# Optimization experiments

Hardware: AMD Instinct MI355X
Metric: run time of the kernel (lower is better)

Reference implementation:

```python
import jax, jax.numpy as jnp
import numpy as np

BETA = 0.25
NUM_CODES = 8192
DIM_LATENT = 256
BATCH = 32768


def setup_inputs() -> dict:
    key = jax.random.key(0)
    k1, k2 = jax.random.split(key)
    z_e = jax.random.normal(k1, (BATCH, DIM_LATENT), dtype=jnp.float32)
    # nn.init.uniform_(codebook.weight, -1/num_codes, 1/num_codes)
    codebook = jax.random.uniform(
        k2, (NUM_CODES, DIM_LATENT), dtype=jnp.float32,
        minval=-1.0 / NUM_CODES, maxval=1.0 / NUM_CODES,
    )
    return {"z_e": z_e, "codebook": codebook}


def reference(z_e, codebook):
    # squared L2 distances via the ||z||^2 + ||e||^2 - 2 z.e expansion
    z2 = jnp.sum(z_e * z_e, axis=1, keepdims=True)          # [B, 1]
    e2 = jnp.sum(codebook * codebook, axis=1)[None, :]       # [1, K]
    ze = jnp.einsum('bd,kd->bk', z_e, codebook)              # [B, K]
    dist = z2 + e2 - 2.0 * ze                                # [B, K]
    indices = jnp.argmin(dist, axis=1)                       # [B]
    z_q = codebook[indices]                                  # [B, d] gather

    cb_loss = jnp.mean((z_q - jax.lax.stop_gradient(z_e)) ** 2)
    commit_loss = jnp.mean((z_e - jax.lax.stop_gradient(z_q)) ** 2)
    vq_loss = cb_loss + BETA * commit_loss

    # straight-through estimator
    z_q_st = z_e + jax.lax.stop_gradient(z_q - z_e)
    return (z_q_st, indices, vq_loss, cb_loss, commit_loss)
```

## Files before the change

### kernel.cpp

```cpp
#include <hip/hip_runtime.h>

#define BATCH   32768
#define DIM     256
#define NCODES  8192
#define BETA    0.25f
#define EPS     3e-4f
#define CAND_CAP 128

typedef unsigned short ushort_t;
typedef unsigned char  uchar_t;
typedef unsigned long long u64;
typedef __attribute__((ext_vector_type(8))) short bf16x8;
typedef __attribute__((ext_vector_type(4))) float f32x4;

#define GLOAD16(gp, lp) __builtin_amdgcn_global_load_lds( \
    (const __attribute__((address_space(1))) void*)(gp), \
    (__attribute__((address_space(3))) void*)(lp), 16, 0, 0)

__device__ inline ushort_t f2bf(float f) {
    union { float f; unsigned u; } v; v.f = f;
    return (ushort_t)((v.u + 0x7FFF + ((v.u >> 16) & 1)) >> 16);
}
__device__ inline ushort_t f2bf_rd(float f) {
    union { float f; unsigned u; } v; v.f = f;
    unsigned u = v.u;
    if (f < 0.0f) u += 0xFFFFu;
    return (ushort_t)(u >> 16);
}

__global__ void vq_prep_kernel(const float* __restrict__ z,
                               const float* __restrict__ cb,
                               float* __restrict__ e2, float* __restrict__ z2,
                               ushort_t* __restrict__ eh, ushort_t* __restrict__ zh,
                               float* __restrict__ loss_acc) {
    const int lane = threadIdx.x & 63;
    const int wid  = threadIdx.x >> 6;
    const int item = blockIdx.x * 4 + wid;
    const float* src;
    ushort_t* dst;
    if (item < NCODES) { src = cb + (size_t)item * DIM;            dst = eh + (size_t)item * DIM; }
    else               { src = z  + (size_t)(item - NCODES) * DIM; dst = zh + (size_t)(item - NCODES) * DIM; }
    const float4 v = *(const float4*)(src + lane * 4);
    ushort4 b; b.x = f2bf(v.x); b.y = f2bf(v.y); b.z = f2bf(v.z); b.w = f2bf(v.w);
    *(ushort4*)(dst + lane * 4) = b;
    float s = v.x * v.x + v.y * v.y + v.z * v.z + v.w * v.w;
    #pragma unroll
    for (int off = 32; off > 0; off >>= 1) s += __shfl_down(s, off, 64);
    if (lane == 0) {
        if (item < NCODES) e2[item] = s;
        else               z2[item - NCODES] = s;
    }
    if (blockIdx.x == 0 && threadIdx.x == 0) *loss_acc = 0.0f;
}

__launch_bounds__(512, 2)
__global__ void vq_screen_kernel(const ushort_t* __restrict__ zh_g,
                                 const ushort_t* __restrict__ eh_g,
                                 const float* __restrict__ e2g,
                                 ushort_t* __restrict__ tilemin_g,
                                 uchar_t* __restrict__ mask_g) {
    __shared__ ushort_t zh_s[2][8 * 512];
    __shared__ ushort_t eh_s[2][32 * 512];

    const int t    = threadIdx.x;
    const int w    = t >> 6;
    const int lane = t & 63;
    const int c    = lane & 15;
    const int q    = lane >> 4;
    const int h    = w >> 2;
    const int cq   = w & 3;
    const int row0 = blockIdx.x * 128;

    #define STAGE(n_, b_) do {                                                 \
        const int ct_ = (n_) >> 3;                                             \
        const int kc_ = ((n_) & 7) * 32;                                       \
        GLOAD16(zh_g + (size_t)(row0 + w * 16 + (lane >> 2)) * DIM + kc_ + (lane & 3) * 8, \
                &zh_s[b_][w * 512]);                                           \
        _Pragma("unroll")                                                      \
        for (int s_ = 0; s_ < 4; ++s_) {                                       \
            const int c16_ = w * 4 + s_;                                       \
            GLOAD16(eh_g + (size_t)(ct_ * 512 + c16_ * 16 + (lane >> 2)) * DIM + kc_ + (lane & 3) * 8, \
                    &eh_s[b_][c16_ * 512]);                                    \
        }                                                                      \
    } while (0)

    STAGE(0, 0);

    f32x4 acc[4][8];
    for (int n = 0; n < 128; ++n) {
        const int kc_i = n & 7;
        if (kc_i == 0) {
            #pragma unroll
            for (int i = 0; i < 4; ++i)
                #pragma unroll
                for (int j = 0; j < 8; ++j) acc[i][j] = (f32x4)0.0f;
        }
        __syncthreads();
        if (n < 127) STAGE(n + 1, (n + 1) & 1);
        const int b = n & 1;

        bf16x8 a[4], bfr[8];
        #pragma unroll
        for (int i = 0; i < 4; ++i)
            a[i] = *(const bf16x8*)&zh_s[b][(h * 4 + i) * 512 + c * 32 + q * 8];
        #pragma unroll
        for (int j = 0; j < 8; ++j)
            bfr[j] = *(const bf16x8*)&eh_s[b][(cq * 8 + j) * 512 + c * 32 + q * 8];
        #pragma unroll
        for (int i = 0; i < 4; ++i)
            #pragma unroll
            for (int j = 0; j < 8; ++j)
                acc[i][j] = __builtin_amdgcn_mfma_f32_16x16x32_bf16(a[i], bfr[j], acc[i][j], 0, 0, 0);

        if (kc_i == 7) {
            const int ct = n >> 3;
            float e2v[8];
            #pragma unroll
            for (int j = 0; j < 8; ++j) e2v[j] = e2g[ct * 512 + cq * 128 + j * 16 + c];

            float tm[4][4];
            #pragma unroll
            for (int i = 0; i < 4; ++i)
                #pragma unroll
                for (int reg = 0; reg < 4; ++reg) tm[i][reg] = 3.4e38f;
            #pragma unroll
            for (int i = 0; i < 4; ++i)
                #pragma unroll
                for (int j = 0; j < 8; ++j)
                    #pragma unroll
                    for (int reg = 0; reg < 4; ++reg) {
                        const float s = fmaf(-2.0f, acc[i][j][reg], e2v[j]);
                        acc[i][j][reg] = s;
                        tm[i][reg] = fminf(tm[i][reg], s);
                    }
            #pragma unroll
            for (int st = 1; st < 16; st <<= 1)
                #pragma unroll
                for (int i = 0; i < 4; ++i)
                    #pragma unroll
                    for (int reg = 0; reg < 4; ++reg)
                        tm[i][reg] = fminf(tm[i][reg], __shfl_xor(tm[i][reg], st, 64));

            const int tile = ct * 4 + cq;
            #pragma unroll
            for (int i = 0; i < 4; ++i)
                #pragma unroll
                for (int reg = 0; reg < 4; ++reg) {
                    const int row = row0 + h * 64 + i * 16 + q * 4 + reg;
                    const float thr = tm[i][reg] + EPS;
                    unsigned m8 = 0;
                    #pragma unroll
                    for (int j = 0; j < 8; ++j)
                        m8 |= (unsigned)(acc[i][j][reg] <= thr) << j;
                    mask_g[(size_t)row * 1024 + tile * 16 + c] = (uchar_t)m8;
                    if (c == 0) tilemin_g[(size_t)row * 64 + tile] = f2bf_rd(tm[i][reg]);
                }
        }
    }
    #undef STAGE
}

__device__ inline u64 vq_eval(const float* zrow, const float* __restrict__ cb,
                              const float* __restrict__ e2g, float z2v, int code) {
    const float4* z4 = (const float4*)zrow;
    const float4* e4 = (const float4*)(cb + (size_t)code * DIM);
    float acc = 0.0f;
    #pragma unroll 8
    for (int k4 = 0; k4 < DIM / 4; ++k4) {
        const float4 a = z4[k4];
        const float4 b = e4[k4];
        acc = fmaf(a.x, b.x, acc);
        acc = fmaf(a.y, b.y, acc);
        acc = fmaf(a.z, b.z, acc);
        acc = fmaf(a.w, b.w, acc);
    }
    const float S  = z2v + e2g[code];
    const float sc = fmaf(-2.0f, acc, S);
    union { float f; unsigned u; } sb; sb.f = sc;
    return ((u64)sb.u << 32) | (unsigned)code;
}

__global__ void vq_select_kernel(const float* __restrict__ z,
                                 const float* __restrict__ cb,
                                 const float* __restrict__ e2g,
                                 const float* __restrict__ z2g,
                                 const ushort_t* __restrict__ tilemin_g,
                                 const uchar_t* __restrict__ mask_g,
                                 float* __restrict__ idx_f,
                                 int* __restrict__ idx_i) {
    __shared__ float    zrow_s[4][DIM];
    __shared__ ushort_t cand_s[4][CAND_CAP];

    const int lane = threadIdx.x & 63;
    const int w    = threadIdx.x >> 6;
    const int row  = blockIdx.x * 4 + w;

    *(float4*)&zrow_s[w][lane * 4] = *(const float4*)(z + (size_t)row * DIM + lane * 4);

    union { unsigned u; float f; } tv;
    tv.u = ((unsigned)tilemin_g[(size_t)row * 64 + lane]) << 16;
    const float tm = tv.f;
    float gmin = tm;
    #pragma unroll
    for (int d = 32; d > 0; d >>= 1) gmin = fminf(gmin, __shfl_xor(gmin, d, 64));
    const float thr = gmin + EPS;

    u64 m0 = 0, m1 = 0;
    if (tm <= thr) {
        const uchar_t* mb = mask_g + (size_t)row * 1024 + lane * 16;
        m0 = *(const u64*)(mb);
        m1 = *(const u64*)(mb + 8);
    }
    const unsigned cnt = __popcll(m0) + __popcll(m1);
    unsigned inc = cnt;
    #pragma unroll
    for (int d = 1; d < 64; d <<= 1) {
        const unsigned o = __shfl_up(inc, d, 64);
        if (lane >= d) inc += o;
    }
    const unsigned excl  = inc - cnt;
    const unsigned total = __shfl(inc, 63, 64);
    const float z2v = z2g[row];
    u64 best = ~0ull;

    __syncthreads();

    unsigned slot = excl;
    while (m0) {
        const int p = __builtin_ctzll(m0); m0 &= m0 - 1;
        const unsigned code = lane * 128 + (p & 7) * 16 + (p >> 3);
        if (slot < CAND_CAP) cand_s[w][slot] = (ushort_t)code;
        else best = min(best, vq_eval(zrow_s[w], cb, e2g, z2v, (int)code));
        ++slot;
    }
    while (m1) {
        const int p = __builtin_ctzll(m1); m1 &= m1 - 1;
        const unsigned code = lane * 128 + (p & 7) * 16 + 8 + (p >> 3);
        if (slot < CAND_CAP) cand_s[w][slot] = (ushort_t)code;
        else best = min(best, vq_eval(zrow_s[w], cb, e2g, z2v, (int)code));
        ++slot;
    }

    __syncthreads();

    const int n = (int)(total < CAND_CAP ? total : CAND_CAP);
    for (int s = lane; s < n; s += 64)
        best = min(best, vq_eval(zrow_s[w], cb, e2g, z2v, (int)cand_s[w][s]));

    #pragma unroll
    for (int d = 32; d > 0; d >>= 1) {
        const u64 o = (u64)__shfl_xor((unsigned long long)best, d, 64);
        best = min(best, o);
    }
    if (lane == 0) {
        const int k = (int)(best & (u64)(NCODES - 1));
        idx_f[row] = (float)k;
        idx_i[row] = k;
    }
}

__global__ void vq_gather_loss_kernel(const float* __restrict__ z,
                                      const float* __restrict__ cb,
                                      const int* __restrict__ idx_i,
                                      float* __restrict__ zq_out,
                                      float* __restrict__ loss_acc) {
    const int lane = threadIdx.x & 63;
    const int wid  = threadIdx.x >> 6;
    const int row  = blockIdx.x * 4 + wid;
    const int k = idx_i[row];
    const float4 e  = *(const float4*)(cb + (size_t)k * DIM + lane * 4);
    const float4 zv = *(const float4*)(z + (size_t)row * DIM + lane * 4);
    const float dx = e.x - zv.x, dy = e.y - zv.y, dz = e.z - zv.z, dw = e.w - zv.w;
    float4 o;
    o.x = zv.x + dx; o.y = zv.y + dy; o.z = zv.z + dz; o.w = zv.w + dw;
    *(float4*)(zq_out + (size_t)row * DIM + lane * 4) = o;
    float s = dx * dx + dy * dy + dz * dz + dw * dw;
    #pragma unroll
    for (int off = 32; off > 0; off >>= 1) s += __shfl_down(s, off, 64);
    __shared__ float wsum[4];
    if (lane == 0) wsum[wid] = s;
    __syncthreads();
    if (threadIdx.x == 0)
        atomicAdd(loss_acc, wsum[0] + wsum[1] + wsum[2] + wsum[3]);
}

__global__ void vq_finalize_kernel(const float* __restrict__ loss_acc,
                                   float* __restrict__ out_losses) {
    const float mean = *loss_acc * (1.0f / (float)(BATCH * DIM));
    out_losses[0] = mean + BETA * mean;
    out_losses[1] = mean;
    out_losses[2] = mean;
}

extern "C" void kernel_launch(void* const* d_in, const int* in_sizes, int n_in,
                              void* d_out, int out_size, void* d_ws, size_t ws_size,
                              hipStream_t stream) {
    const float* z  = (const float*)d_in[0];
    const float* cb = (const float*)d_in[1];

    float* out    = (float*)d_out;
    float* zq     = out;
    float* idx_f  = out + (size_t)BATCH * DIM;
    float* losses = out + (size_t)BATCH * DIM + BATCH;
    uchar_t* mask = (uchar_t*)d_out;

    float*    ws        = (float*)d_ws;
    float*    loss_acc  = ws;
    float*    e2        = ws + 256;
    float*    z2        = e2 + NCODES;
    ushort_t* tilemin   = (ushort_t*)(z2 + BATCH);
    int*      idxi      = (int*)(tilemin + (size_t)BATCH * 64);
    ushort_t* zh        = (ushort_t*)(idxi + BATCH);
    ushort_t* eh        = zh + (size_t)BATCH * DIM;

    vq_prep_kernel<<<(NCODES + BATCH) / 4, 256, 0, stream>>>(z, cb, e2, z2, eh, zh, loss_acc);
    vq_screen_kernel<<<BATCH / 128, 512, 0, stream>>>(zh, eh, e2, tilemin, mask);
    vq_select_kernel<<<BATCH / 4, 256, 0, stream>>>(z, cb, e2, z2, tilemin, mask, idx_f, idxi);
    vq_gather_loss_kernel<<<BATCH / 4, 256, 0, stream>>>(z, cb, idxi, zq, loss_acc);
    vq_finalize_kernel<<<1, 1, 0, stream>>>(loss_acc, losses);
}
```

Baseline: 497.3 us.

## Stage screen tiles via registers with fragment-ordered LDS layout instead of global_load_lds

```diff
diff --git a/kernel.cpp b/kernel.cpp
--- a/kernel.cpp
+++ b/kernel.cpp
@@ -12,10 +12,6 @@
 typedef unsigned long long u64;
 typedef __attribute__((ext_vector_type(8))) short bf16x8;
 typedef __attribute__((ext_vector_type(4))) float f32x4;
-
-#define GLOAD16(gp, lp) __builtin_amdgcn_global_load_lds( \
-    (const __attribute__((address_space(1))) void*)(gp), \
-    (__attribute__((address_space(3))) void*)(lp), 16, 0, 0)
 
 __device__ inline ushort_t f2bf(float f) {
     union { float f; unsigned u; } v; v.f = f;
@@ -70,42 +66,49 @@
     const int h    = w >> 2;
     const int cq   = w & 3;
     const int row0 = blockIdx.x * 128;
-
-    #define STAGE(n_, b_) do {                                                 \
+    const int srow = lane & 15;
+    const int skc  = (lane >> 4) * 8;
+
+    #define LOADC(n_) do {                                                     \
         const int ct_ = (n_) >> 3;                                             \
         const int kc_ = ((n_) & 7) * 32;                                       \
-        GLOAD16(zh_g + (size_t)(row0 + w * 16 + (lane >> 2)) * DIM + kc_ + (lane & 3) * 8, \
-                &zh_s[b_][w * 512]);                                           \
+        rz = *(const int4*)(zh_g + (size_t)(row0 + w * 16 + srow) * DIM + kc_ + skc); \
         _Pragma("unroll")                                                      \
-        for (int s_ = 0; s_ < 4; ++s_) {                                       \
-            const int c16_ = w * 4 + s_;                                       \
-            GLOAD16(eh_g + (size_t)(ct_ * 512 + c16_ * 16 + (lane >> 2)) * DIM + kc_ + (lane & 3) * 8, \
-                    &eh_s[b_][c16_ * 512]);                                    \
-        }                                                                      \
+        for (int s_ = 0; s_ < 4; ++s_)                                         \
+            re[s_] = *(const int4*)(eh_g + (size_t)(ct_ * 512 + (w * 4 + s_) * 16 + srow) * DIM + kc_ + skc); \
     } while (0)
-
-    STAGE(0, 0);
+    #define WRITEC(b_) do {                                                    \
+        *(int4*)&zh_s[b_][w * 512 + lane * 8] = rz;                            \
+        _Pragma("unroll")                                                      \
+        for (int s_ = 0; s_ < 4; ++s_)                                         \
+            *(int4*)&eh_s[b_][(w * 4 + s_) * 512 + lane * 8] = re[s_];         \
+    } while (0)
+
+    int4 rz, re[4];
+    LOADC(0);
+    WRITEC(0);
+    __syncthreads();
 
     f32x4 acc[4][8];
     for (int n = 0; n < 128; ++n) {
         const int kc_i = n & 7;
+        const int b = n & 1;
         if (kc_i == 0) {
             #pragma unroll
             for (int i = 0; i < 4; ++i)
                 #pragma unroll
                 for (int j = 0; j < 8; ++j) acc[i][j] = (f32x4)0.0f;
         }
-        __syncthreads();
-        if (n < 127) STAGE(n + 1, (n + 1) & 1);
-        const int b = n & 1;
+
+        if (n < 127) LOADC(n + 1);
 
         bf16x8 a[4], bfr[8];
         #pragma unroll
         for (int i = 0; i < 4; ++i)
-            a[i] = *(const bf16x8*)&zh_s[b][(h * 4 + i) * 512 + c * 32 + q * 8];
+            a[i] = *(const bf16x8*)&zh_s[b][(h * 4 + i) * 512 + lane * 8];
         #pragma unroll
         for (int j = 0; j < 8; ++j)
-            bfr[j] = *(const bf16x8*)&eh_s[b][(cq * 8 + j) * 512 + c * 32 + q * 8];
+            bfr[j] = *(const bf16x8*)&eh_s[b][(cq * 8 + j) * 512 + lane * 8];
         #pragma unroll
         for (int i = 0; i < 4; ++i)
             #pragma unroll
@@ -156,8 +159,12 @@
                     if (c == 0) tilemin_g[(size_t)row * 64 + tile] = f2bf_rd(tm[i][reg]);
                 }
         }
-    }
-    #undef STAGE
+
+        if (n < 127) WRITEC(b ^ 1);
+        __syncthreads();
+    }
+    #undef LOADC
+    #undef WRITEC
 }
 
 __device__ inline u64 vq_eval(const float* zrow, const float* __restrict__ cb,
```

Result: slower. 674.3 us (+35.6%).

## Keep z tile resident in LDS for screen; fuse gather-loss into select

Applied to the files above, without the earlier changes.

```diff
diff --git a/kernel.cpp b/kernel.cpp
--- a/kernel.cpp
+++ b/kernel.cpp
@@ -59,7 +59,7 @@
                                  const float* __restrict__ e2g,
                                  ushort_t* __restrict__ tilemin_g,
                                  uchar_t* __restrict__ mask_g) {
-    __shared__ ushort_t zh_s[2][8 * 512];
+    __shared__ ushort_t zh_s[64 * 512];
     __shared__ ushort_t eh_s[2][32 * 512];
 
     const int t    = threadIdx.x;
@@ -70,20 +70,24 @@
     const int h    = w >> 2;
     const int cq   = w & 3;
     const int row0 = blockIdx.x * 128;
+    const int srow = lane & 15;
+    const int skc  = (lane >> 4) * 8;
 
     #define STAGE(n_, b_) do {                                                 \
         const int ct_ = (n_) >> 3;                                             \
         const int kc_ = ((n_) & 7) * 32;                                       \
-        GLOAD16(zh_g + (size_t)(row0 + w * 16 + (lane >> 2)) * DIM + kc_ + (lane & 3) * 8, \
-                &zh_s[b_][w * 512]);                                           \
         _Pragma("unroll")                                                      \
         for (int s_ = 0; s_ < 4; ++s_) {                                       \
             const int c16_ = w * 4 + s_;                                       \
-            GLOAD16(eh_g + (size_t)(ct_ * 512 + c16_ * 16 + (lane >> 2)) * DIM + kc_ + (lane & 3) * 8, \
+            GLOAD16(eh_g + (size_t)(ct_ * 512 + c16_ * 16 + srow) * DIM + kc_ + skc, \
                     &eh_s[b_][c16_ * 512]);                                    \
         }                                                                      \
     } while (0)
 
+    #pragma unroll
+    for (int rt = 0; rt < 8; ++rt)
+        GLOAD16(zh_g + (size_t)(row0 + rt * 16 + srow) * DIM + w * 32 + skc,
+                &zh_s[(w * 8 + rt) * 512]);
     STAGE(0, 0);
 
     f32x4 acc[4][8];
@@ -102,10 +106,10 @@
         bf16x8 a[4], bfr[8];
         #pragma unroll
         for (int i = 0; i < 4; ++i)
-            a[i] = *(const bf16x8*)&zh_s[b][(h * 4 + i) * 512 + c * 32 + q * 8];
+            a[i] = *(const bf16x8*)&zh_s[(kc_i * 8 + h * 4 + i) * 512 + lane * 8];
         #pragma unroll
         for (int j = 0; j < 8; ++j)
-            bfr[j] = *(const bf16x8*)&eh_s[b][(cq * 8 + j) * 512 + c * 32 + q * 8];
+            bfr[j] = *(const bf16x8*)&eh_s[b][(cq * 8 + j) * 512 + lane * 8];
         #pragma unroll
         for (int i = 0; i < 4; ++i)
             #pragma unroll
@@ -187,9 +191,11 @@
                                  const ushort_t* __restrict__ tilemin_g,
                                  const uchar_t* __restrict__ mask_g,
                                  float* __restrict__ idx_f,
-                                 int* __restrict__ idx_i) {
+                                 float* __restrict__ zq_out,
+                                 float* __restrict__ loss_acc) {
     __shared__ float    zrow_s[4][DIM];
     __shared__ ushort_t cand_s[4][CAND_CAP];
+    __shared__ float    wsum[4];
 
     const int lane = threadIdx.x & 63;
     const int w    = threadIdx.x >> 6;
@@ -252,24 +258,11 @@
         const u64 o = (u64)__shfl_xor((unsigned long long)best, d, 64);
         best = min(best, o);
     }
-    if (lane == 0) {
-        const int k = (int)(best & (u64)(NCODES - 1));
-        idx_f[row] = (float)k;
-        idx_i[row] = k;
-    }
-}
-
-__global__ void vq_gather_loss_kernel(const float* __restrict__ z,
-                                      const float* __restrict__ cb,
-                                      const int* __restrict__ idx_i,
-                                      float* __restrict__ zq_out,
-                                      float* __restrict__ loss_acc) {
-    const int lane = threadIdx.x & 63;
-    const int wid  = threadIdx.x >> 6;
-    const int row  = blockIdx.x * 4 + wid;
-    const int k = idx_i[row];
+    const int k = (int)(best & (u64)(NCODES - 1));
+    if (lane == 0) idx_f[row] = (float)k;
+
     const float4 e  = *(const float4*)(cb + (size_t)k * DIM + lane * 4);
-    const float4 zv = *(const float4*)(z + (size_t)row * DIM + lane * 4);
+    const float4 zv = *(const float4*)&zrow_s[w][lane * 4];
     const float dx = e.x - zv.x, dy = e.y - zv.y, dz = e.z - zv.z, dw = e.w - zv.w;
     float4 o;
     o.x = zv.x + dx; o.y = zv.y + dy; o.z = zv.z + dz; o.w = zv.w + dw;
@@ -277,8 +270,7 @@
     float s = dx * dx + dy * dy + dz * dz + dw * dw;
     #pragma unroll
     for (int off = 32; off > 0; off >>= 1) s += __shfl_down(s, off, 64);
-    __shared__ float wsum[4];
-    if (lane == 0) wsum[wid] = s;
+    if (lane == 0) wsum[w] = s;
     __syncthreads();
     if (threadIdx.x == 0)
         atomicAdd(loss_acc, wsum[0] + wsum[1] + wsum[2] + wsum[3]);
@@ -309,13 +301,11 @@
     float*    e2        = ws + 256;
     float*    z2        = e2 + NCODES;
     ushort_t* tilemin   = (ushort_t*)(z2 + BATCH);
-    int*      idxi      = (int*)(tilemin + (size_t)BATCH * 64);
-    ushort_t* zh        = (ushort_t*)(idxi + BATCH);
+    ushort_t* zh        = tilemin + (size_t)BATCH * 64;
     ushort_t* eh        = zh + (size_t)BATCH * DIM;
 
     vq_prep_kernel<<<(NCODES + BATCH) / 4, 256, 0, stream>>>(z, cb, e2, z2, eh, zh, loss_acc);
     vq_screen_kernel<<<BATCH / 128, 512, 0, stream>>>(zh, eh, e2, tilemin, mask);
-    vq_select_kernel<<<BATCH / 4, 256, 0, stream>>>(z, cb, e2, z2, tilemin, mask, idx_f, idxi);
-    vq_gather_loss_kernel<<<BATCH / 4, 256, 0, stream>>>(z, cb, idxi, zq, loss_acc);
+    vq_select_kernel<<<BATCH / 4, 256, 0, stream>>>(z, cb, e2, z2, tilemin, mask, idx_f, zq, loss_acc);
     vq_finalize_kernel<<<1, 1, 0, stream>>>(loss_acc, losses);
 }
```

After: 467.7 us. -5.9%, faster.
